# Optimization experiments

Measured on AMD Instinct MI355X. Metric: run time of the kernel, lower is better.

The kernel has to match this reference:

```python
import jax, jax.numpy as jnp
import numpy as np

E = 32  # embed_dim
B = 524288


def _mha(q_tok, kv_tok, Wi, bi, Wo, bo):
    """Single-head torch-style MultiheadAttention (batch_first).
    Wi: [3E, E] packed q/k/v in_proj; Wo: [E, E] out_proj.
    q_tok: [B, Lq, E], kv_tok: [B, Lk, E].
    """
    Wq, Wk, Wv = Wi[:E], Wi[E:2 * E], Wi[2 * E:]
    bq, bk, bv = bi[:E], bi[E:2 * E], bi[2 * E:]
    q = q_tok @ Wq.T + bq
    k = kv_tok @ Wk.T + bk
    v = kv_tok @ Wv.T + bv
    scores = jnp.einsum('bqd,bkd->bqk', q, k) / jnp.sqrt(jnp.asarray(E, q.dtype))
    attn = jax.nn.softmax(scores, axis=-1)
    out = jnp.einsum('bqk,bkd->bqd', attn, v)
    return out @ Wo.T + bo


def setup_inputs() -> dict:
    key = jax.random.key(0)
    ks = jax.random.split(key, 14)
    s = 0.1
    return {
        'groupA_feats': jax.random.normal(ks[0], (B, 3), jnp.float32),
        'groupB_feats': jax.random.normal(ks[1], (B, 2), jnp.float32),
        'WA': jax.random.normal(ks[2], (E, 1), jnp.float32) * s,
        'bA': jax.random.normal(ks[3], (E,), jnp.float32) * s,
        'WB': jax.random.normal(ks[4], (E, 1), jnp.float32) * s,
        'bB': jax.random.normal(ks[5], (E,), jnp.float32) * s,
        'Wi_AB': jax.random.normal(ks[6], (3 * E, E), jnp.float32) * s,
        'bi_AB': jax.random.normal(ks[7], (3 * E,), jnp.float32) * s,
        'Wo_AB': jax.random.normal(ks[8], (E, E), jnp.float32) * s,
        'bo_AB': jnp.zeros((E,), jnp.float32),
        'Wi_BA': jax.random.normal(ks[9], (3 * E, E), jnp.float32) * s,
        'bi_BA': jax.random.normal(ks[10], (3 * E,), jnp.float32) * s,
        'Wo_BA': jax.random.normal(ks[11], (E, E), jnp.float32) * s,
        'bo_BA': jnp.zeros((E,), jnp.float32),
        'Wf': jax.random.normal(ks[12], (1, E), jnp.float32) * s,
        'bf': jax.random.normal(ks[13], (1,), jnp.float32) * s,
    }


def reference(groupA_feats, groupB_feats, WA, bA, WB, bB,
              Wi_AB, bi_AB, Wo_AB, bo_AB, Wi_BA, bi_BA, Wo_BA, bo_BA,
              Wf, bf):
    # Per-feature Linear(1, E) embeddings, vectorized over the feature dim:
    # A_tokens[b, i, :] = groupA[b, i] * WA[:, 0] + bA
    A_tokens = groupA_feats[:, :, None] * WA[:, 0][None, None, :] + bA  # [B,3,E]
    B_tokens = groupB_feats[:, :, None] * WB[:, 0][None, None, :] + bB  # [B,2,E]
    crossAB = _mha(A_tokens, B_tokens, Wi_AB, bi_AB, Wo_AB, bo_AB)      # [B,3,E]
    crossBA = _mha(B_tokens, A_tokens, Wi_BA, bi_BA, Wo_BA, bo_BA)      # [B,2,E]
    combined = (crossAB.mean(axis=1) + crossBA.mean(axis=1)) * 0.5       # [B,E]
    out = combined @ Wf.T + bf                                           # [B,1]
    return jnp.where(out >= 0, out, 0.01 * out)  # LeakyReLU(0.01)
```

## Files before the change

### kernel.cpp

```cpp
#include <hip/hip_runtime.h>
#include <math.h>


__global__ void precompute_consts(
    const float* __restrict__ WA, const float* __restrict__ bA,
    const float* __restrict__ WB, const float* __restrict__ bB,
    const float* __restrict__ WiAB, const float* __restrict__ biAB,
    const float* __restrict__ WoAB, const float* __restrict__ boAB,
    const float* __restrict__ WiBA, const float* __restrict__ biBA,
    const float* __restrict__ WoBA, const float* __restrict__ boBA,
    const float* __restrict__ Wf, const float* __restrict__ bf,
    float* __restrict__ consts)
{
    __shared__ float uq[2][32], uk[2][32], cq[2][32], uv[2][32], cv[2][32];
    __shared__ float p[2][32], r[2][32];
    const int e = threadIdx.x;
    if (e < 32) {
        float s_uq = 0.f, s_uk = 0.f, s_cq = 0.f, s_uv = 0.f, s_cv = 0.f;
        for (int d = 0; d < 32; ++d) {
            const float wq = WiAB[e * 32 + d];
            const float wk = WiAB[(32 + e) * 32 + d];
            const float wv = WiAB[(64 + e) * 32 + d];
            s_uq += wq * WA[d];
            s_cq += wq * bA[d];
            s_uk += wk * WB[d];
            s_uv += wv * WB[d];
            s_cv += wv * bB[d];
        }
        uq[0][e] = s_uq; uk[0][e] = s_uk; cq[0][e] = s_cq + biAB[e];
        uv[0][e] = s_uv; cv[0][e] = s_cv + biAB[64 + e];

        s_uq = 0.f; s_uk = 0.f; s_cq = 0.f; s_uv = 0.f; s_cv = 0.f;
        for (int d = 0; d < 32; ++d) {
            const float wq = WiBA[e * 32 + d];
            const float wk = WiBA[(32 + e) * 32 + d];
            const float wv = WiBA[(64 + e) * 32 + d];
            s_uq += wq * WB[d];
            s_cq += wq * bB[d];
            s_uk += wk * WA[d];
            s_uv += wv * WA[d];
            s_cv += wv * bA[d];
        }
        uq[1][e] = s_uq; uk[1][e] = s_uk; cq[1][e] = s_cq + biBA[e];
        uv[1][e] = s_uv; cv[1][e] = s_cv + biBA[64 + e];
    }
    __syncthreads();
    if (e < 32) {
        float pAB = 0.f, rAB = 0.f, pBA = 0.f, rBA = 0.f;
        for (int d = 0; d < 32; ++d) {
            pAB += WoAB[e * 32 + d] * uv[0][d];
            rAB += WoAB[e * 32 + d] * cv[0][d];
            pBA += WoBA[e * 32 + d] * uv[1][d];
            rBA += WoBA[e * 32 + d] * cv[1][d];
        }
        p[0][e] = pAB; r[0][e] = rAB + boAB[e];
        p[1][e] = pBA; r[1][e] = rBA + boBA[e];
    }
    __syncthreads();
    if (e == 0) {
        float aAB = 0.f, gAB = 0.f, aBA = 0.f, gBA = 0.f;
        float c1 = 0.f, c2 = 0.f, c0 = 0.f;
        for (int d = 0; d < 32; ++d) {
            aAB += uq[0][d] * uk[0][d];
            gAB += cq[0][d] * uk[0][d];
            aBA += uq[1][d] * uk[1][d];
            gBA += cq[1][d] * uk[1][d];
            c1  += Wf[d] * p[0][d];
            c2  += Wf[d] * p[1][d];
            c0  += Wf[d] * (r[0][d] + r[1][d]);
        }
        const float inv_sqrt_e = 0.17677669529663688f;
        consts[0] = aAB * inv_sqrt_e;
        consts[1] = gAB * inv_sqrt_e;
        consts[2] = aBA * inv_sqrt_e;
        consts[3] = gBA * inv_sqrt_e;
        consts[4] = 0.5f * c0 + bf[0];
        consts[5] = 0.5f * c1;
        consts[6] = 0.5f * c2;
    }
}

__device__ __forceinline__ float sigmoidf_(float x) {
    return 1.0f / (1.0f + expf(-x));
}

__global__ void fused_main(const float* __restrict__ Af,
                           const float* __restrict__ Bf,
                           const float* __restrict__ consts,
                           float* __restrict__ out, int n)
{
    const float kaAB = consts[0], kgAB = consts[1];
    const float kaBA = consts[2], kgBA = consts[3];
    const float c0 = consts[4], c1 = consts[5], c2 = consts[6];

    const int i = blockIdx.x * blockDim.x + threadIdx.x;
    if (i >= n) return;

    const float a0 = Af[3 * i + 0];
    const float a1 = Af[3 * i + 1];
    const float a2 = Af[3 * i + 2];
    const float2 bb = *reinterpret_cast<const float2*>(Bf + 2 * i);
    const float b0 = bb.x, b1 = bb.y;

    const float dB = b0 - b1;
    const float s0 = b1 + dB * sigmoidf_(dB * (kaAB * a0 + kgAB));
    const float s1 = b1 + dB * sigmoidf_(dB * (kaAB * a1 + kgAB));
    const float s2 = b1 + dB * sigmoidf_(dB * (kaAB * a2 + kgAB));
    const float S_AB = (s0 + s1 + s2) * (1.0f / 3.0f);

    float S_BA = 0.f;
    #pragma unroll
    for (int j = 0; j < 2; ++j) {
        const float bj = (j == 0) ? b0 : b1;
        const float c = kaBA * bj + kgBA;
        const float l0 = a0 * c, l1 = a1 * c, l2 = a2 * c;
        const float m = fmaxf(l0, fmaxf(l1, l2));
        const float e0 = expf(l0 - m), e1 = expf(l1 - m), e2 = expf(l2 - m);
        S_BA += (e0 * a0 + e1 * a1 + e2 * a2) / (e0 + e1 + e2);
    }
    S_BA *= 0.5f;

    const float y = c0 + c1 * S_AB + c2 * S_BA;
    out[i] = (y >= 0.f) ? y : 0.01f * y;
}

extern "C" void kernel_launch(void* const* d_in, const int* in_sizes, int n_in,
                              void* d_out, int out_size, void* d_ws, size_t ws_size,
                              hipStream_t stream) {
    const float* groupA = (const float*)d_in[0];
    const float* groupB = (const float*)d_in[1];
    const float* WA   = (const float*)d_in[2];
    const float* bA   = (const float*)d_in[3];
    const float* WB   = (const float*)d_in[4];
    const float* bB   = (const float*)d_in[5];
    const float* WiAB = (const float*)d_in[6];
    const float* biAB = (const float*)d_in[7];
    const float* WoAB = (const float*)d_in[8];
    const float* boAB = (const float*)d_in[9];
    const float* WiBA = (const float*)d_in[10];
    const float* biBA = (const float*)d_in[11];
    const float* WoBA = (const float*)d_in[12];
    const float* boBA = (const float*)d_in[13];
    const float* Wf   = (const float*)d_in[14];
    const float* bf   = (const float*)d_in[15];

    float* out = (float*)d_out;
    float* consts = (float*)d_ws;

    const int n = in_sizes[0] / 3;

    precompute_consts<<<1, 64, 0, stream>>>(
        WA, bA, WB, bB, WiAB, biAB, WoAB, boAB,
        WiBA, biBA, WoBA, boBA, Wf, bf, consts);

    const int block = 256;
    const int grid = (n + block - 1) / block;
    fused_main<<<grid, block, 0, stream>>>(groupA, groupB, consts, out, n);
}
```

Measured before the change: 96.92 us.

## Fuse constant precompute into main kernel and process four rows per thread

Removes the separate single-block precompute launch by having every block recompute the folded attention constants in shared memory, using 64 threads and a shuffle reduction. The main pass now handles four rows per thread with float4 vector loads and stores. This drops one launch and its serial dependency, but every one of the 512 blocks redoes about 3K weight loads and FMAs before its element work. The grid also shrinks fourfold, which lowers the number of waves available to hide latency.

```diff
diff --git a/kernel.cpp b/kernel.cpp
--- a/kernel.cpp
+++ b/kernel.cpp
@@ -2,7 +2,40 @@
 #include <math.h>
 
 
-__global__ void precompute_consts(
+__device__ __forceinline__ float sigmoidf_(float x) {
+    return 1.0f / (1.0f + expf(-x));
+}
+
+__device__ __forceinline__ float one_elem(
+    float a0, float a1, float a2, float b0, float b1,
+    float kaAB, float kgAB, float kaBA, float kgBA,
+    float c0, float c1, float c2)
+{
+    const float dB = b0 - b1;
+    const float s0 = b1 + dB * sigmoidf_(dB * fmaf(kaAB, a0, kgAB));
+    const float s1 = b1 + dB * sigmoidf_(dB * fmaf(kaAB, a1, kgAB));
+    const float s2 = b1 + dB * sigmoidf_(dB * fmaf(kaAB, a2, kgAB));
+    const float S_AB = (s0 + s1 + s2) * (1.0f / 3.0f);
+
+    float S_BA = 0.f;
+    #pragma unroll
+    for (int j = 0; j < 2; ++j) {
+        const float bj = (j == 0) ? b0 : b1;
+        const float c = fmaf(kaBA, bj, kgBA);
+        const float l0 = a0 * c, l1 = a1 * c, l2 = a2 * c;
+        const float m = fmaxf(l0, fmaxf(l1, l2));
+        const float e0 = expf(l0 - m), e1 = expf(l1 - m), e2 = expf(l2 - m);
+        S_BA += (e0 * a0 + e1 * a1 + e2 * a2) / (e0 + e1 + e2);
+    }
+    S_BA *= 0.5f;
+
+    const float y = fmaf(c1, S_AB, fmaf(c2, S_BA, c0));
+    return (y >= 0.f) ? y : 0.01f * y;
+}
+
+__global__ __launch_bounds__(256) void fused_all(
+    const float* __restrict__ Af,
+    const float* __restrict__ Bf,
     const float* __restrict__ WA, const float* __restrict__ bA,
     const float* __restrict__ WB, const float* __restrict__ bB,
     const float* __restrict__ WiAB, const float* __restrict__ biAB,
@@ -10,118 +43,125 @@
     const float* __restrict__ WiBA, const float* __restrict__ biBA,
     const float* __restrict__ WoBA, const float* __restrict__ boBA,
     const float* __restrict__ Wf, const float* __restrict__ bf,
-    float* __restrict__ consts)
+    float* __restrict__ out, int n)
 {
     __shared__ float uq[2][32], uk[2][32], cq[2][32], uv[2][32], cv[2][32];
     __shared__ float p[2][32], r[2][32];
-    const int e = threadIdx.x;
-    if (e < 32) {
+    __shared__ float cst[7];
+
+    const int tid = threadIdx.x;
+
+    if (tid < 64) {
+        const int s = tid >> 5;
+        const int e = tid & 31;
+        const float* Wi     = s ? WiBA : WiAB;
+        const float* bi     = s ? biBA : biAB;
+        const float* wq_vec = s ? WB : WA;
+        const float* bq_vec = s ? bB : bA;
+        const float* wk_vec = s ? WA : WB;
+        const float* bk_vec = s ? bA : bB;
         float s_uq = 0.f, s_uk = 0.f, s_cq = 0.f, s_uv = 0.f, s_cv = 0.f;
+        #pragma unroll
         for (int d = 0; d < 32; ++d) {
-            const float wq = WiAB[e * 32 + d];
-            const float wk = WiAB[(32 + e) * 32 + d];
-            const float wv = WiAB[(64 + e) * 32 + d];
-            s_uq += wq * WA[d];
-            s_cq += wq * bA[d];
-            s_uk += wk * WB[d];
-            s_uv += wv * WB[d];
-            s_cv += wv * bB[d];
+            const float wq = Wi[e * 32 + d];
+            const float wk = Wi[(32 + e) * 32 + d];
+            const float wv = Wi[(64 + e) * 32 + d];
+            s_uq += wq * wq_vec[d];
+            s_cq += wq * bq_vec[d];
+            s_uk += wk * wk_vec[d];
+            s_uv += wv * wk_vec[d];
+            s_cv += wv * bk_vec[d];
         }
-        uq[0][e] = s_uq; uk[0][e] = s_uk; cq[0][e] = s_cq + biAB[e];
-        uv[0][e] = s_uv; cv[0][e] = s_cv + biAB[64 + e];
-
-        s_uq = 0.f; s_uk = 0.f; s_cq = 0.f; s_uv = 0.f; s_cv = 0.f;
-        for (int d = 0; d < 32; ++d) {
-            const float wq = WiBA[e * 32 + d];
-            const float wk = WiBA[(32 + e) * 32 + d];
-            const float wv = WiBA[(64 + e) * 32 + d];
-            s_uq += wq * WB[d];
-            s_cq += wq * bB[d];
-            s_uk += wk * WA[d];
-            s_uv += wv * WA[d];
-            s_cv += wv * bA[d];
-        }
-        uq[1][e] = s_uq; uk[1][e] = s_uk; cq[1][e] = s_cq + biBA[e];
-        uv[1][e] = s_uv; cv[1][e] = s_cv + biBA[64 + e];
+        uq[s][e] = s_uq; uk[s][e] = s_uk;
+        cq[s][e] = s_cq + bi[e];
+        uv[s][e] = s_uv; cv[s][e] = s_cv + bi[64 + e];
     }
     __syncthreads();
-    if (e < 32) {
-        float pAB = 0.f, rAB = 0.f, pBA = 0.f, rBA = 0.f;
+
+    if (tid < 64) {
+        const int s = tid >> 5;
+        const int e = tid & 31;
+        const float* Wo = s ? WoBA : WoAB;
+        const float* bo = s ? boBA : boAB;
+        float sp = 0.f, sr = 0.f;
+        #pragma unroll
         for (int d = 0; d < 32; ++d) {
-            pAB += WoAB[e * 32 + d] * uv[0][d];
-            rAB += WoAB[e * 32 + d] * cv[0][d];
-            pBA += WoBA[e * 32 + d] * uv[1][d];
-            rBA += WoBA[e * 32 + d] * cv[1][d];
+            const float w = Wo[e * 32 + d];
+            sp += w * uv[s][d];
+            sr += w * cv[s][d];
         }
-        p[0][e] = pAB; r[0][e] = rAB + boAB[e];
-        p[1][e] = pBA; r[1][e] = rBA + boBA[e];
+        p[s][e] = sp; r[s][e] = sr + bo[e];
     }
     __syncthreads();
-    if (e == 0) {
-        float aAB = 0.f, gAB = 0.f, aBA = 0.f, gBA = 0.f;
-        float c1 = 0.f, c2 = 0.f, c0 = 0.f;
-        for (int d = 0; d < 32; ++d) {
-            aAB += uq[0][d] * uk[0][d];
-            gAB += cq[0][d] * uk[0][d];
-            aBA += uq[1][d] * uk[1][d];
-            gBA += cq[1][d] * uk[1][d];
-            c1  += Wf[d] * p[0][d];
-            c2  += Wf[d] * p[1][d];
-            c0  += Wf[d] * (r[0][d] + r[1][d]);
+
+    if (tid < 32) {
+        const int d = tid;
+        float vaAB = uq[0][d] * uk[0][d];
+        float vgAB = cq[0][d] * uk[0][d];
+        float vaBA = uq[1][d] * uk[1][d];
+        float vgBA = cq[1][d] * uk[1][d];
+        const float wf = Wf[d];
+        float vc1 = wf * p[0][d];
+        float vc2 = wf * p[1][d];
+        float vc0 = wf * (r[0][d] + r[1][d]);
+        #pragma unroll
+        for (int off = 16; off > 0; off >>= 1) {
+            vaAB += __shfl_down(vaAB, off, 32);
+            vgAB += __shfl_down(vgAB, off, 32);
+            vaBA += __shfl_down(vaBA, off, 32);
+            vgBA += __shfl_down(vgBA, off, 32);
+            vc1  += __shfl_down(vc1,  off, 32);
+            vc2  += __shfl_down(vc2,  off, 32);
+            vc0  += __shfl_down(vc0,  off, 32);
         }
-        const float inv_sqrt_e = 0.17677669529663688f;
-        consts[0] = aAB * inv_sqrt_e;
-        consts[1] = gAB * inv_sqrt_e;
-        consts[2] = aBA * inv_sqrt_e;
-        consts[3] = gBA * inv_sqrt_e;
-        consts[4] = 0.5f * c0 + bf[0];
-        consts[5] = 0.5f * c1;
-        consts[6] = 0.5f * c2;
+        if (d == 0) {
+            const float inv_sqrt_e = 0.17677669529663688f;
+            cst[0] = vaAB * inv_sqrt_e;
+            cst[1] = vgAB * inv_sqrt_e;
+            cst[2] = vaBA * inv_sqrt_e;
+            cst[3] = vgBA * inv_sqrt_e;
+            cst[4] = 0.5f * vc0 + bf[0];
+            cst[5] = 0.5f * vc1;
+            cst[6] = 0.5f * vc2;
+        }
     }
-}
+    __syncthreads();
 
-__device__ __forceinline__ float sigmoidf_(float x) {
-    return 1.0f / (1.0f + expf(-x));
-}
+    const float kaAB = cst[0], kgAB = cst[1];
+    const float kaBA = cst[2], kgBA = cst[3];
+    const float c0 = cst[4], c1 = cst[5], c2 = cst[6];
 
-__global__ void fused_main(const float* __restrict__ Af,
-                           const float* __restrict__ Bf,
-                           const float* __restrict__ consts,
-                           float* __restrict__ out, int n)
-{
-    const float kaAB = consts[0], kgAB = consts[1];
-    const float kaBA = consts[2], kgBA = consts[3];
-    const float c0 = consts[4], c1 = consts[5], c2 = consts[6];
+    const int q = blockIdx.x * blockDim.x + tid;
+    const int base = q * 4;
 
-    const int i = blockIdx.x * blockDim.x + threadIdx.x;
-    if (i >= n) return;
+    if (base + 3 < n) {
+        const float4 af0 = *reinterpret_cast<const float4*>(Af + 3 * base);
+        const float4 af1 = *reinterpret_cast<const float4*>(Af + 3 * base + 4);
+        const float4 af2 = *reinterpret_cast<const float4*>(Af + 3 * base + 8);
+        const float4 bf0 = *reinterpret_cast<const float4*>(Bf + 2 * base);
+        const float4 bf1 = *reinterpret_cast<const float4*>(Bf + 2 * base + 4);
 
-    const float a0 = Af[3 * i + 0];
-    const float a1 = Af[3 * i + 1];
-    const float a2 = Af[3 * i + 2];
-    const float2 bb = *reinterpret_cast<const float2*>(Bf + 2 * i);
-    const float b0 = bb.x, b1 = bb.y;
-
-    const float dB = b0 - b1;
-    const float s0 = b1 + dB * sigmoidf_(dB * (kaAB * a0 + kgAB));
-    const float s1 = b1 + dB * sigmoidf_(dB * (kaAB * a1 + kgAB));
-    const float s2 = b1 + dB * sigmoidf_(dB * (kaAB * a2 + kgAB));
-    const float S_AB = (s0 + s1 + s2) * (1.0f / 3.0f);
-
-    float S_BA = 0.f;
-    #pragma unroll
-    for (int j = 0; j < 2; ++j) {
-        const float bj = (j == 0) ? b0 : b1;
-        const float c = kaBA * bj + kgBA;
-        const float l0 = a0 * c, l1 = a1 * c, l2 = a2 * c;
-        const float m = fmaxf(l0, fmaxf(l1, l2));
-        const float e0 = expf(l0 - m), e1 = expf(l1 - m), e2 = expf(l2 - m);
-        S_BA += (e0 * a0 + e1 * a1 + e2 * a2) / (e0 + e1 + e2);
+        float4 o;
+        o.x = one_elem(af0.x, af0.y, af0.z, bf0.x, bf0.y,
+                       kaAB, kgAB, kaBA, kgBA, c0, c1, c2);
+        o.y = one_elem(af0.w, af1.x, af1.y, bf0.z, bf0.w,
+                       kaAB, kgAB, kaBA, kgBA, c0, c1, c2);
+        o.z = one_elem(af1.z, af1.w, af2.x, bf1.x, bf1.y,
+                       kaAB, kgAB, kaBA, kgBA, c0, c1, c2);
+        o.w = one_elem(af2.y, af2.z, af2.w, bf1.z, bf1.w,
+                       kaAB, kgAB, kaBA, kgBA, c0, c1, c2);
+        *reinterpret_cast<float4*>(out + base) = o;
+    } else {
+        for (int i = base; i < n; ++i) {
+            const float a0 = Af[3 * i + 0];
+            const float a1 = Af[3 * i + 1];
+            const float a2 = Af[3 * i + 2];
+            const float b0 = Bf[2 * i + 0];
+            const float b1 = Bf[2 * i + 1];
+            out[i] = one_elem(a0, a1, a2, b0, b1,
+                              kaAB, kgAB, kaBA, kgBA, c0, c1, c2);
+        }
     }
-    S_BA *= 0.5f;
-
-    const float y = c0 + c1 * S_AB + c2 * S_BA;
-    out[i] = (y >= 0.f) ? y : 0.01f * y;
 }
 
 extern "C" void kernel_launch(void* const* d_in, const int* in_sizes, int n_in,
@@ -145,15 +185,14 @@
     const float* bf   = (const float*)d_in[15];
 
     float* out = (float*)d_out;
-    float* consts = (float*)d_ws;
-
     const int n = in_sizes[0] / 3;
 
-    precompute_consts<<<1, 64, 0, stream>>>(
-        WA, bA, WB, bB, WiAB, biAB, WoAB, boAB,
-        WiBA, biBA, WoBA, boBA, Wf, bf, consts);
+    const int block = 256;
+    const int nq = (n + 3) >> 2;
+    const int grid = (nq + block - 1) / block;
 
-    const int block = 256;
-    const int grid = (n + block - 1) / block;
-    fused_main<<<grid, block, 0, stream>>>(groupA, groupB, consts, out, n);
+    fused_all<<<grid, block, 0, stream>>>(
+        groupA, groupB, WA, bA, WB, bB,
+        WiAB, biAB, WoAB, boAB, WiBA, biBA, WoBA, boBA,
+        Wf, bf, out, n);
 }
```

After: 93.58 us. 3.4% less time.
